# Performance work log

Measured on AMD Instinct MI355X. Metric: run time of the kernel, lower is better.

Reference implementation:

```python
import jax, jax.numpy as jnp
import numpy as np

NBATCH, NUP, NDOWN, NMO, NCONF = 8192, 8, 8, 32, 64


def setup_inputs() -> dict:
    key = jax.random.key(0)
    k1, k2, k3, k4 = jax.random.split(key, 4)
    MO = jax.random.normal(k1, (NBATCH, NUP + NDOWN, NMO), dtype=jnp.float32)
    d2MO = jax.random.normal(k2, (NBATCH, NUP + NDOWN, NMO), dtype=jnp.float32)
    # each config = 8 distinct MO column indices per spin (distinct -> invertible A)
    configs_up = jnp.argsort(jax.random.uniform(k3, (NCONF, NMO)), axis=1)[:, :NUP].astype(jnp.int32)
    configs_down = jnp.argsort(jax.random.uniform(k4, (NCONF, NMO)), axis=1)[:, :NDOWN].astype(jnp.int32)
    return {"MO": MO, "d2MO": d2MO, "configs_up": configs_up, "configs_down": configs_down}


def _gather(M, elec_idx, cols):
    # M: (B, nelec, nmo) -> select electron rows then per-config MO columns
    Ms = M[:, elec_idx, :]                  # (B, n, nmo)
    A = jnp.take(Ms, cols, axis=2)          # (B, n, C, n)
    return jnp.transpose(A, (0, 2, 1, 3))   # (B, C, n, n)


def reference(MO, d2MO, configs_up, configs_down):
    nup = configs_up.shape[1]
    ndown = configs_down.shape[1]
    iup = jnp.arange(nup)
    idown = jnp.arange(nup, nup + ndown)

    Aup = _gather(MO, iup, configs_up)       # (B, C, nup, nup)
    Adn = _gather(MO, idown, configs_down)   # (B, C, ndown, ndown)
    d2up = _gather(d2MO, iup, configs_up)
    d2dn = _gather(d2MO, idown, configs_down)

    iAup = jnp.linalg.inv(Aup)
    iAdn = jnp.linalg.inv(Adn)

    # btrace(iA @ d2A) = sum_ij iA[i,j] * d2A[j,i]
    tr = lambda X, Y: jnp.einsum('bcij,bcji->bc', X, Y)
    out = tr(iAup, d2up) + tr(iAdn, d2dn)    # (B, C)

    # return_local_energy=False branch: multiply by product of determinants
    pd = jnp.linalg.det(Aup) * jnp.linalg.det(Adn)
    return -0.5 * out * pd
```

## Files before the change

### kernel.cpp

```cpp
#include <hip/hip_runtime.h>

#define NBATCH 8192
#define NELEC  16
#define NMO    32
#define NCONF  64
#define NS     8
#define TSTR   20
#define TSZ    (NMO * TSTR)

typedef float v2f __attribute__((ext_vector_type(2)));

__device__ __forceinline__ v2f pkfma(v2f a, v2f b, v2f c) {
#if __has_builtin(__builtin_elementwise_fma)
    return __builtin_elementwise_fma(a, b, c);
#else
    return a * b + c;
#endif
}
__device__ __forceinline__ v2f bc2(float s) { return (v2f){s, s}; }
__device__ __forceinline__ float getel2(const v2f (&R)[4], int j) {
    return (j & 1) ? R[j >> 1].y : R[j >> 1].x;
}
__device__ __forceinline__ void setel2(v2f (&R)[4], int j, float v) {
    if (j & 1) R[j >> 1].y = v; else R[j >> 1].x = v;
}

__device__ __forceinline__ void solve8T(const float* __restrict__ MOT,
                                        const float* __restrict__ D2T,
                                        const int (&cols)[NS], int eoff,
                                        float& det_out, float& tr_out)
{
    v2f A2[NS][4];
    #pragma unroll
    for (int j = 0; j < NS; ++j) {
        const float4* pa = (const float4*)(MOT + cols[j] * TSTR + eoff);
        float4 a0 = pa[0], a1 = pa[1];
        A2[j][0] = (v2f){a0.x, a0.y};
        A2[j][1] = (v2f){a0.z, a0.w};
        A2[j][2] = (v2f){a1.x, a1.y};
        A2[j][3] = (v2f){a1.z, a1.w};
    }

    float det = 1.0f;
    #pragma unroll
    for (int k = 0; k < NS; ++k) {
        float ukk = getel2(A2[k], k);
        det *= ukk;
        float pinv = __builtin_amdgcn_rcpf(ukk);
        #pragma unroll
        for (int r = k + 1; r < NS; ++r) {
            float m = getel2(A2[r], k) * pinv;
            v2f m2 = bc2(m);
            #pragma unroll
            for (int p = (k + 1) >> 1; p < 4; ++p)
                A2[r][p] = pkfma(-m2, A2[k][p], A2[r][p]);
            setel2(A2[r], k, m);
        }
        setel2(A2[k], k, pinv);
    }

    float tr = 0.0f;
    #pragma unroll
    for (int t = 0; t < 4; ++t) {
        const int k0 = 2 * t, k1 = 2 * t + 1;

        const float4* pd0 = (const float4*)(D2T + cols[k0] * TSTR + eoff);
        const float4* pd1 = (const float4*)(D2T + cols[k1] * TSTR + eoff);
        float4 d00 = pd0[0], d01 = pd0[1];
        float4 d10 = pd1[0], d11 = pd1[1];
        const float dk0[NS] = {d00.x, d00.y, d00.z, d00.w, d01.x, d01.y, d01.z, d01.w};
        const float dk1[NS] = {d10.x, d10.y, d10.z, d10.w, d11.x, d11.y, d11.z, d11.w};

        v2f y2[NS];
        y2[k0] = (v2f){1.0f, 0.0f};
        y2[k1] = (v2f){-getel2(A2[k1], k0), 1.0f};
        #pragma unroll
        for (int i = k1 + 1; i < NS; ++i) {
            v2f acc = (v2f){0.0f, 0.0f};
            #pragma unroll
            for (int j = k0; j < i; ++j)
                acc = pkfma(bc2(getel2(A2[i], j)), y2[j], acc);
            y2[i] = -acc;
        }

        v2f x2[NS];
        #pragma unroll
        for (int i = NS - 1; i >= 0; --i) {
            v2f acc = (i >= k0) ? y2[i] : (v2f){0.0f, 0.0f};
            #pragma unroll
            for (int c2 = i + 1; c2 < NS; ++c2)
                acc = pkfma(-bc2(getel2(A2[i], c2)), x2[c2], acc);
            x2[i] = acc * bc2(getel2(A2[i], i));
        }

        #pragma unroll
        for (int i = 0; i < NS; ++i) {
            tr = fmaf(x2[i].x, dk0[i], tr);
            tr = fmaf(x2[i].y, dk1[i], tr);
        }
    }

    det_out = det;
    tr_out  = tr;
}

__global__ __launch_bounds__(256)
void kp_pk_kernel(const float* __restrict__ MO,
                  const float* __restrict__ d2MO,
                  const int*   __restrict__ cfg_up,
                  const int*   __restrict__ cfg_dn,
                  float*       __restrict__ out)
{
    __shared__ float smem[2][2][TSZ];

    const int tid  = threadIdx.x;
    const int half = tid >> 7;
    const int u    = tid & 127;
    const int b    = blockIdx.x * 2 + half;

    float* MOT = smem[half][0];
    float* D2T = smem[half][1];

    const float* MOb = MO   + (size_t)b * NELEC * NMO;
    const float* d2b = d2MO + (size_t)b * NELEC * NMO;

    {
        int r = u >> 3;
        int c = (u & 7) * 4;
        float4 v = *(const float4*)(MOb + r * NMO + c);
        float4 w = *(const float4*)(d2b + r * NMO + c);
        MOT[(c + 0) * TSTR + r] = v.x;
        MOT[(c + 1) * TSTR + r] = v.y;
        MOT[(c + 2) * TSTR + r] = v.z;
        MOT[(c + 3) * TSTR + r] = v.w;
        D2T[(c + 0) * TSTR + r] = w.x;
        D2T[(c + 1) * TSTR + r] = w.y;
        D2T[(c + 2) * TSTR + r] = w.z;
        D2T[(c + 3) * TSTR + r] = w.w;
    }
    __syncthreads();

    const int cidx = u >> 1;
    const int s    = u & 1;
    const int* cfg = s ? cfg_dn : cfg_up;
    int4 c0 = ((const int4*)cfg)[cidx * 2 + 0];
    int4 c1 = ((const int4*)cfg)[cidx * 2 + 1];
    const int cols[NS] = {c0.x, c0.y, c0.z, c0.w, c1.x, c1.y, c1.z, c1.w};

    float det, tr;
    solve8T(MOT, D2T, cols, s * NS, det, tr);

    float det_o = __shfl_xor(det, 1);
    float tr_o  = __shfl_xor(tr, 1);
    if (s == 0)
        out[(size_t)b * NCONF + cidx] = -0.5f * (tr + tr_o) * det * det_o;
}

extern "C" void kernel_launch(void* const* d_in, const int* in_sizes, int n_in,
                              void* d_out, int out_size, void* d_ws, size_t ws_size,
                              hipStream_t stream)
{
    const float* MO     = (const float*)d_in[0];
    const float* d2MO   = (const float*)d_in[1];
    const int*   cfg_up = (const int*)d_in[2];
    const int*   cfg_dn = (const int*)d_in[3];
    float* out = (float*)d_out;

    dim3 grid(NBATCH / 2);
    dim3 block(256);
    kp_pk_kernel<<<grid, block, 0, stream>>>(MO, d2MO, cfg_up, cfg_dn, out);
}
```

Baseline: 89.73 us.

## Process four batches per block with double-buffered LDS prefetch

Each 128-thread block now handles four batch elements strided by the grid size. It prefetches the next batch's MO and d2MO rows into registers while solving the current one, then writes them into a second LDS buffer. This hides global-load latency, amortizes the config loads and block launch cost, and cuts the grid to 2048 blocks. In exchange it gives fewer resident waves for latency hiding and adds an extra barrier per iteration.

```diff
diff --git a/kernel.cpp b/kernel.cpp
--- a/kernel.cpp
+++ b/kernel.cpp
@@ -7,6 +7,8 @@
 #define NS     8
 #define TSTR   20
 #define TSZ    (NMO * TSTR)
+#define NBPB   4
+#define GRIDN  (NBATCH / NBPB)
 
 typedef float v2f __attribute__((ext_vector_type(2)));
 
@@ -104,56 +106,75 @@
     tr_out  = tr;
 }
 
-__global__ __launch_bounds__(256)
-void kp_pk_kernel(const float* __restrict__ MO,
-                  const float* __restrict__ d2MO,
-                  const int*   __restrict__ cfg_up,
-                  const int*   __restrict__ cfg_dn,
-                  float*       __restrict__ out)
+__global__ __launch_bounds__(128)
+void kp_persist_kernel(const float* __restrict__ MO,
+                       const float* __restrict__ d2MO,
+                       const int*   __restrict__ cfg_up,
+                       const int*   __restrict__ cfg_dn,
+                       float*       __restrict__ out)
 {
     __shared__ float smem[2][2][TSZ];
 
-    const int tid  = threadIdx.x;
-    const int half = tid >> 7;
-    const int u    = tid & 127;
-    const int b    = blockIdx.x * 2 + half;
-
-    float* MOT = smem[half][0];
-    float* D2T = smem[half][1];
-
-    const float* MOb = MO   + (size_t)b * NELEC * NMO;
-    const float* d2b = d2MO + (size_t)b * NELEC * NMO;
-
-    {
-        int r = u >> 3;
-        int c = (u & 7) * 4;
-        float4 v = *(const float4*)(MOb + r * NMO + c);
-        float4 w = *(const float4*)(d2b + r * NMO + c);
-        MOT[(c + 0) * TSTR + r] = v.x;
-        MOT[(c + 1) * TSTR + r] = v.y;
-        MOT[(c + 2) * TSTR + r] = v.z;
-        MOT[(c + 3) * TSTR + r] = v.w;
-        D2T[(c + 0) * TSTR + r] = w.x;
-        D2T[(c + 1) * TSTR + r] = w.y;
-        D2T[(c + 2) * TSTR + r] = w.z;
-        D2T[(c + 3) * TSTR + r] = w.w;
-    }
-    __syncthreads();
+    const int u = threadIdx.x;
+    const int r = u >> 3;
+    const int c = (u & 7) * 4;
 
     const int cidx = u >> 1;
     const int s    = u & 1;
     const int* cfg = s ? cfg_dn : cfg_up;
-    int4 c0 = ((const int4*)cfg)[cidx * 2 + 0];
-    int4 c1 = ((const int4*)cfg)[cidx * 2 + 1];
-    const int cols[NS] = {c0.x, c0.y, c0.z, c0.w, c1.x, c1.y, c1.z, c1.w};
+    int4 cc0 = ((const int4*)cfg)[cidx * 2 + 0];
+    int4 cc1 = ((const int4*)cfg)[cidx * 2 + 1];
+    const int cols[NS] = {cc0.x, cc0.y, cc0.z, cc0.w, cc1.x, cc1.y, cc1.z, cc1.w};
 
-    float det, tr;
-    solve8T(MOT, D2T, cols, s * NS, det, tr);
+    int b = blockIdx.x;
+    {
+        const float* MOb = MO   + (size_t)b * NELEC * NMO;
+        const float* d2b = d2MO + (size_t)b * NELEC * NMO;
+        float4 v = *(const float4*)(MOb + r * NMO + c);
+        float4 w = *(const float4*)(d2b + r * NMO + c);
+        float* MOT = smem[0][0];
+        float* D2T = smem[0][1];
+        MOT[(c + 0) * TSTR + r] = v.x;  MOT[(c + 1) * TSTR + r] = v.y;
+        MOT[(c + 2) * TSTR + r] = v.z;  MOT[(c + 3) * TSTR + r] = v.w;
+        D2T[(c + 0) * TSTR + r] = w.x;  D2T[(c + 1) * TSTR + r] = w.y;
+        D2T[(c + 2) * TSTR + r] = w.z;  D2T[(c + 3) * TSTR + r] = w.w;
+    }
+    __syncthreads();
 
-    float det_o = __shfl_xor(det, 1);
-    float tr_o  = __shfl_xor(tr, 1);
-    if (s == 0)
-        out[(size_t)b * NCONF + cidx] = -0.5f * (tr + tr_o) * det * det_o;
+    int cur = 0;
+    #pragma unroll
+    for (int it = 0; it < NBPB; ++it) {
+        const bool more = (it + 1 < NBPB);
+
+        float4 vn, wn;
+        if (more) {
+            const float* MOn = MO   + (size_t)(b + GRIDN) * NELEC * NMO;
+            const float* d2n = d2MO + (size_t)(b + GRIDN) * NELEC * NMO;
+            vn = *(const float4*)(MOn + r * NMO + c);
+            wn = *(const float4*)(d2n + r * NMO + c);
+        }
+
+        {
+            float det, tr;
+            solve8T(smem[cur][0], smem[cur][1], cols, s * NS, det, tr);
+            float det_o = __shfl_xor(det, 1);
+            float tr_o  = __shfl_xor(tr, 1);
+            if (s == 0)
+                out[(size_t)b * NCONF + cidx] = -0.5f * (tr + tr_o) * det * det_o;
+        }
+
+        if (more) {
+            float* MOT = smem[cur ^ 1][0];
+            float* D2T = smem[cur ^ 1][1];
+            MOT[(c + 0) * TSTR + r] = vn.x;  MOT[(c + 1) * TSTR + r] = vn.y;
+            MOT[(c + 2) * TSTR + r] = vn.z;  MOT[(c + 3) * TSTR + r] = vn.w;
+            D2T[(c + 0) * TSTR + r] = wn.x;  D2T[(c + 1) * TSTR + r] = wn.y;
+            D2T[(c + 2) * TSTR + r] = wn.z;  D2T[(c + 3) * TSTR + r] = wn.w;
+            __syncthreads();
+            cur ^= 1;
+            b += GRIDN;
+        }
+    }
 }
 
 extern "C" void kernel_launch(void* const* d_in, const int* in_sizes, int n_in,
@@ -166,7 +187,7 @@
     const int*   cfg_dn = (const int*)d_in[3];
     float* out = (float*)d_out;
 
-    dim3 grid(NBATCH / 2);
-    dim3 block(256);
-    kp_pk_kernel<<<grid, block, 0, stream>>>(MO, d2MO, cfg_up, cfg_dn, out);
+    dim3 grid(GRIDN);
+    dim3 block(128);
+    kp_persist_kernel<<<grid, block, 0, stream>>>(MO, d2MO, cfg_up, cfg_dn, out);
 }
```

Result: slower. 92.98 us (+3.6%).
